# Optimization experiments

Measured on AMD Instinct MI355X. Metric: run time of the kernel, lower is better.

The kernel has to match this reference:

```python
import jax, jax.numpy as jnp
import numpy as np
import math

B, T, C, H = 2, 2048, 1024, 16

def setup_inputs() -> dict:
    key = jax.random.key(0)
    ks = jax.random.split(key, 5)
    s = 0.02
    return {
        "x": jax.random.normal(ks[0], (B, T, C), dtype=jnp.float32),
        "W_attn": jax.random.normal(ks[1], (C, 3 * C), dtype=jnp.float32) * s,
        "b_attn": jnp.zeros((3 * C,), dtype=jnp.float32),
        "W_proj": jax.random.normal(ks[2], (C, C), dtype=jnp.float32) * s,
        "b_proj": jnp.zeros((C,), dtype=jnp.float32),
    }

def reference(x, W_attn, b_attn, W_proj, b_proj):
    Bx, Tx, Cx = x.shape
    hd = Cx // H  # head dim = 64
    qkv = x @ W_attn + b_attn                      # [B,T,3C]
    q, k, v = jnp.split(qkv, 3, axis=-1)
    # [B,H,T,hd]
    q = q.reshape(Bx, Tx, H, hd).transpose(0, 2, 1, 3)
    k = k.reshape(Bx, Tx, H, hd).transpose(0, 2, 1, 3)
    v = v.reshape(Bx, Tx, H, hd).transpose(0, 2, 1, 3)
    scale = 1.0 / math.sqrt(hd)
    att = jnp.einsum('bhqd,bhkd->bhqk', q, k) * scale   # [B,H,T,T]
    causal = jnp.tril(jnp.ones((Tx, Tx), dtype=bool))
    att = jnp.where(causal[None, None, :, :], att, -jnp.inf)
    att = jax.nn.softmax(att, axis=-1)
    y = jnp.einsum('bhqk,bhkd->bhqd', att, v)           # [B,H,T,hd]
    y = y.transpose(0, 2, 1, 3).reshape(Bx, Tx, Cx)
    return y @ W_proj + b_proj
```

## Files before the change

### kernel.cpp

```cpp
#include <hip/hip_runtime.h>

typedef __attribute__((ext_vector_type(8))) __bf16 bf16x8;
typedef __attribute__((ext_vector_type(4))) float f32x4;

#define T_SEQ 2048
#define NH 16
#define HD 64
#define CDIM 1024
#define NQK 2048
#define NQKV 3072
#define MTOT 4096

#define SWZ(r, c) ((((r) * 8) + ((c) ^ ((r) & 7))) * 8)

__device__ __forceinline__ void async_load16(const void* g, void* l) {
    __builtin_amdgcn_global_load_lds(
        (const __attribute__((address_space(1))) void*)g,
        (__attribute__((address_space(3))) void*)l, 16, 0, 0);
}

__device__ __forceinline__ unsigned cvtpk_bf16(float lo, float hi) {
    unsigned r;
    asm("v_cvt_pk_bf16_f32 %0, %1, %2" : "=v"(r) : "v"(lo), "v"(hi));
    return r;
}
__device__ __forceinline__ void swap32(unsigned& a, unsigned& b) {
    asm("v_permlane32_swap_b32 %0, %1" : "+v"(a), "+v"(b));
}
__device__ __forceinline__ void swap16(unsigned& a, unsigned& b) {
    asm("v_permlane16_swap_b32 %0, %1" : "+v"(a), "+v"(b));
}

__global__ __launch_bounds__(256) void prep_kernel(
    const float* __restrict__ x, __bf16* __restrict__ xb,
    const float* __restrict__ Wa, const float* __restrict__ Wp,
    __bf16* __restrict__ WaT, __bf16* __restrict__ WpT) {
    __shared__ float tile[32][33];
    int bid = blockIdx.x;
    if (bid < 2048) {
        int i = (bid * 256 + threadIdx.x) * 8;
        float4 f0 = *(const float4*)(x + i);
        float4 f1 = *(const float4*)(x + i + 4);
        bf16x8 o;
        o[0] = (__bf16)f0.x; o[1] = (__bf16)f0.y; o[2] = (__bf16)f0.z; o[3] = (__bf16)f0.w;
        o[4] = (__bf16)f1.x; o[5] = (__bf16)f1.y; o[6] = (__bf16)f1.z; o[7] = (__bf16)f1.w;
        *(bf16x8*)(xb + i) = o;
        return;
    }
    int fb = bid - 2048;
    int bx = fb & 127, by = fb >> 7;
    const float* in; __bf16* out; int C;
    if (bx < 96) { in = Wa; out = WaT; C = 3072; }
    else         { in = Wp; out = WpT; C = 1024; bx -= 96; }
    int c0 = bx * 32, r0 = by * 32;
    int tx = threadIdx.x & 31, ty = threadIdx.x >> 5;
#pragma unroll
    for (int i = 0; i < 4; i++)
        tile[ty + i * 8][tx] = in[(size_t)(r0 + ty + i * 8) * C + c0 + tx];
    __syncthreads();
#pragma unroll
    for (int i = 0; i < 4; i++)
        out[(size_t)(c0 + ty + i * 8) * 1024 + r0 + tx] = (__bf16)tile[tx][ty + i * 8];
}

template <int WNW>
__global__ __launch_bounds__(256) void gemm_bt_kernel(
    const __bf16* __restrict__ A, const __bf16* __restrict__ Bt,
    const float* __restrict__ bias, int M, int N, int K, int mode,
    __bf16* __restrict__ qkb, __bf16* __restrict__ vtb, float* __restrict__ outf)
{
    constexpr int MI = (WNW == 2) ? 4 : 2;
    constexpr int BROWS = WNW * 64;
    __shared__ __bf16 As[128 * 64];
    __shared__ __bf16 Bs[BROWS * 64];

    int tid = threadIdx.x;
    int lane = tid & 63, wid = tid >> 6;
    int quad = lane >> 4, r16 = lane & 15;
    int wm = (WNW == 2) ? (wid >> 1) * 64 : wid * 32;
    int wn = (WNW == 2) ? (wid & 1) * 64 : 0;

    int id = blockIdx.y * gridDim.x + blockIdx.x;
    int nx = gridDim.x, ny = gridDim.y;
    int xcd = id & 7, wi = id >> 3;
    int cpx = nx >> 1;
    int rpx = ny >> 2;
    int rr = wi / cpx, cc = wi - rr * cpx;
    int bys = (xcd >> 1) * rpx + rr;
    int bxs = (xcd & 1) * cpx + cc;
    int bm = bys * 128, bn = bxs * (WNW * 64);

    f32x4 acc[MI][4] = {};

    int lrow = lane >> 3;
    int lcolsw = (((lane & 7) ^ (lrow & 7)) * 8);
    const __bf16* Ag = A + (size_t)(bm + wid * 32 + lrow) * K + lcolsw;
    const __bf16* Bg = Bt + (size_t)(bn + wid * (BROWS / 4) + lrow) * K + lcolsw;
    char* lA = (char*)As + wid * 4096;
    char* lB = (char*)Bs + wid * (BROWS / 4) * 128;

    for (int kt = 0; kt < K; kt += 64) {
        __syncthreads();
#pragma unroll
        for (int i = 0; i < 4; i++)
            async_load16(Ag + kt + (size_t)i * 8 * K, lA + i * 1024);
#pragma unroll
        for (int i = 0; i < BROWS / 32; i++)
            async_load16(Bg + kt + (size_t)i * 8 * K, lB + i * 1024);
        __syncthreads();
#pragma unroll
        for (int ks = 0; ks < 2; ks++) {
            bf16x8 af[MI], bfr[4];
#pragma unroll
            for (int i = 0; i < MI; i++)
                af[i] = *(const bf16x8*)&As[SWZ(wm + i * 16 + r16, ks * 4 + quad)];
#pragma unroll
            for (int i = 0; i < 4; i++)
                bfr[i] = *(const bf16x8*)&Bs[SWZ(wn + i * 16 + r16, ks * 4 + quad)];
#pragma unroll
            for (int mi = 0; mi < MI; mi++)
#pragma unroll
                for (int ni = 0; ni < 4; ni++)
                    acc[mi][ni] = __builtin_amdgcn_mfma_f32_16x16x32_bf16(
                        af[mi], bfr[ni], acc[mi][ni], 0, 0, 0);
        }
    }

    const float SC2 = 0.125f * 1.44269504088896f;
#pragma unroll
    for (int mi = 0; mi < MI; mi++) {
#pragma unroll
        for (int ni = 0; ni < 4; ni++) {
            int col = bn + wn + ni * 16 + r16;
            float bv = bias[col];
            int row0 = bm + wm + mi * 16 + quad * 4;
            if (mode == 1) {
#pragma unroll
                for (int rg = 0; rg < 4; rg++)
                    outf[(size_t)(row0 + rg) * N + col] = acc[mi][ni][rg] + bv;
            } else if (col < 1024) {
#pragma unroll
                for (int rg = 0; rg < 4; rg++)
                    qkb[(size_t)(row0 + rg) * NQK + col] = (__bf16)((acc[mi][ni][rg] + bv) * SC2);
            } else if (col < 2048) {
#pragma unroll
                for (int rg = 0; rg < 4; rg++)
                    qkb[(size_t)(row0 + rg) * NQK + col] = (__bf16)(acc[mi][ni][rg] + bv);
            } else {
                int dcol = col - 2048;
                int b = row0 >> 11, t0 = row0 & 2047;
                union { __bf16 h[4]; uint2 u; } pk;
#pragma unroll
                for (int rg = 0; rg < 4; rg++) pk.h[rg] = (__bf16)(acc[mi][ni][rg] + bv);
                *(uint2*)&vtb[((size_t)b * 1024 + dcol) * T_SEQ + t0] = pk.u;
            }
        }
    }
}

__global__ __launch_bounds__(256) void attn_kernel(
    const __bf16* __restrict__ qkb, const __bf16* __restrict__ vtb,
    __bf16* __restrict__ y1)
{
    __shared__ __bf16 Ks[2][64 * 64];
    __shared__ __bf16 Vs[2][64 * 64];

    int tid = threadIdx.x;
    int lane = tid & 63, w = tid >> 6;
    int quad = lane >> 4, r16 = lane & 15;
    int bh = blockIdx.y;
    int b = bh >> 4, h = bh & 15;
    int qtA = blockIdx.x, qtB = 31 - blockIdx.x;
    int qbA = qtA * 64, qbB = qtB * 64;

    const __bf16* Qh = qkb + (size_t)b * T_SEQ * NQK + h * HD;
    const __bf16* Kh = Qh + CDIM;
    const __bf16* Vh = vtb + ((size_t)b * 1024 + h * HD) * T_SEQ;

    const float NEG_INF = -__builtin_inff();
    int lrow = lane >> 3;
    int lcolsw = (((lane & 7) ^ (lrow & 7)) * 8);

    bf16x8 qfA[2], qfB[2];
#pragma unroll
    for (int ks = 0; ks < 2; ks++) {
        qfA[ks] = *(const bf16x8*)(Qh + (size_t)(qbA + w * 16 + r16) * NQK + ks * 32 + quad * 8);
        qfB[ks] = *(const bf16x8*)(Qh + (size_t)(qbB + w * 16 + r16) * NQK + ks * 32 + quad * 8);
    }

    bf16x8 onesv;
#pragma unroll
    for (int i = 0; i < 8; i++) onesv[i] = (__bf16)1.0f;

    f32x4 oA[4] = {}, oB[4] = {};
    f32x4 lA4 = {}, lB4 = {};
    int g0A = qbA + w * 16, g0B = qbB + w * 16;
    int qrowA = g0A + r16, qrowB = g0B + r16;

    auto stage = [&](int kt, int buf) {
        int kb = kt * 64;
        char* lK = (char*)Ks[buf] + w * 2048;
        char* lV = (char*)Vs[buf] + w * 2048;
        const __bf16* kg = Kh + (size_t)(kb + w * 16 + lrow) * NQK + lcolsw;
        const __bf16* vg = Vh + (size_t)(w * 16 + lrow) * T_SEQ + kb + lcolsw;
        async_load16(kg, lK);
        async_load16(kg + (size_t)8 * NQK, lK + 1024);
        async_load16(vg, lV);
        async_load16(vg + (size_t)8 * T_SEQ, lV + 1024);
    };

    auto softmax_xchg = [&](f32x4 (&s)[4], int qrow, int kb, bool diag,
                            bf16x8 (&pb)[2]) {
        if (diag) {
#pragma unroll
            for (int ni = 0; ni < 4; ni++)
#pragma unroll
                for (int rg = 0; rg < 4; rg++)
                    if (kb + ni * 16 + quad * 4 + rg > qrow) s[ni][rg] = NEG_INF;
        }
#pragma unroll
        for (int ni = 0; ni < 4; ni++)
#pragma unroll
            for (int rg = 0; rg < 4; rg++)
                s[ni][rg] = __builtin_amdgcn_exp2f(s[ni][rg]);
#pragma unroll
        for (int ks = 0; ks < 2; ks++) {
            unsigned X0 = cvtpk_bf16(s[2 * ks][0], s[2 * ks][1]);
            unsigned X1 = cvtpk_bf16(s[2 * ks][2], s[2 * ks][3]);
            unsigned Y0 = cvtpk_bf16(s[2 * ks + 1][0], s[2 * ks + 1][1]);
            unsigned Y1 = cvtpk_bf16(s[2 * ks + 1][2], s[2 * ks + 1][3]);
            swap32(X0, Y0); swap16(X0, Y0);
            swap32(X1, Y1); swap16(X1, Y1);
            union { unsigned u[4]; bf16x8 v; } pk;
            pk.u[0] = X0; pk.u[1] = X1; pk.u[2] = Y0; pk.u[3] = Y1;
            pb[ks] = pk.v;
        }
    };

    int nktA = qtA + 1, nktB = qtB + 1;
    stage(0, 0);
    int cur = 0;
    for (int kt = 0; kt < nktB; kt++) {
        __syncthreads();
        if (kt + 1 < nktB) stage(kt + 1, cur ^ 1);
        const bool doA = (kt < nktA);
        const int kb = kt * 64;

        f32x4 sB[4] = {}, sA[4] = {};
#pragma unroll
        for (int ks = 0; ks < 2; ks++) {
            bf16x8 kf[4];
#pragma unroll
            for (int ni = 0; ni < 4; ni++)
                kf[ni] = *(const bf16x8*)&Ks[cur][SWZ(ni * 16 + r16, ks * 4 + quad)];
            __builtin_amdgcn_s_setprio(1);
#pragma unroll
            for (int ni = 0; ni < 4; ni++)
                sB[ni] = __builtin_amdgcn_mfma_f32_16x16x32_bf16(kf[ni], qfB[ks], sB[ni], 0, 0, 0);
            if (doA) {
#pragma unroll
                for (int ni = 0; ni < 4; ni++)
                    sA[ni] = __builtin_amdgcn_mfma_f32_16x16x32_bf16(kf[ni], qfA[ks], sA[ni], 0, 0, 0);
            }
            __builtin_amdgcn_s_setprio(0);
        }

        bf16x8 pbB[2], pbA[2];
        softmax_xchg(sB, qrowB, kb, kb + 63 > g0B, pbB);
        if (doA) softmax_xchg(sA, qrowA, kb, kb + 63 > g0A, pbA);

#pragma unroll
        for (int ks = 0; ks < 2; ks++) {
            bf16x8 vf[4];
#pragma unroll
            for (int nd = 0; nd < 4; nd++)
                vf[nd] = *(const bf16x8*)&Vs[cur][SWZ(nd * 16 + r16, ks * 4 + quad)];
            __builtin_amdgcn_s_setprio(1);
#pragma unroll
            for (int nd = 0; nd < 4; nd++)
                oB[nd] = __builtin_amdgcn_mfma_f32_16x16x32_bf16(vf[nd], pbB[ks], oB[nd], 0, 0, 0);
            lB4 = __builtin_amdgcn_mfma_f32_16x16x32_bf16(onesv, pbB[ks], lB4, 0, 0, 0);
            __builtin_amdgcn_s_setprio(0);
            if (doA) {
                __builtin_amdgcn_s_setprio(1);
#pragma unroll
                for (int nd = 0; nd < 4; nd++)
                    oA[nd] = __builtin_amdgcn_mfma_f32_16x16x32_bf16(vf[nd], pbA[ks], oA[nd], 0, 0, 0);
                lA4 = __builtin_amdgcn_mfma_f32_16x16x32_bf16(onesv, pbA[ks], lA4, 0, 0, 0);
                __builtin_amdgcn_s_setprio(0);
            }
        }
        cur ^= 1;
    }

#pragma unroll
    for (int which = 0; which < 2; which++) {
        f32x4* o = which ? oB : oA;
        float inv = 1.f / (which ? lB4[0] : lA4[0]);
        int t = (which ? qbB : qbA) + w * 16 + r16;
#pragma unroll
        for (int nd = 0; nd < 4; nd++) {
            union { __bf16 h4[4]; uint2 u; } pk;
#pragma unroll
            for (int rg = 0; rg < 4; rg++) pk.h4[rg] = (__bf16)(o[nd][rg] * inv);
            *(uint2*)&y1[(size_t)(b * T_SEQ + t) * CDIM + h * HD + nd * 16 + quad * 4] = pk.u;
        }
    }
}

extern "C" void kernel_launch(void* const* d_in, const int* in_sizes, int n_in,
                              void* d_out, int out_size, void* d_ws, size_t ws_size,
                              hipStream_t stream) {
    const float* x = (const float*)d_in[0];
    const float* W_attn = (const float*)d_in[1];
    const float* b_attn = (const float*)d_in[2];
    const float* W_proj = (const float*)d_in[3];
    const float* b_proj = (const float*)d_in[4];
    float* out = (float*)d_out;

    char* p = (char*)d_ws;
    __bf16* xb = (__bf16*)p;   p += (size_t)MTOT * CDIM * 2;
    __bf16* WaT = (__bf16*)p;  p += (size_t)3 * CDIM * CDIM * 2;
    __bf16* WpT = (__bf16*)p;  p += (size_t)CDIM * CDIM * 2;
    __bf16* qkb = (__bf16*)p;  p += (size_t)MTOT * NQK * 2;
    __bf16* vtb = (__bf16*)p;  p += (size_t)2 * 1024 * T_SEQ * 2;
    __bf16* y1 = xb;

    prep_kernel<<<2048 + 4096, 256, 0, stream>>>(x, xb, W_attn, W_proj, WaT, WpT);
    gemm_bt_kernel<2><<<dim3(24, 32), 256, 0, stream>>>(xb, WaT, b_attn, MTOT, NQKV, CDIM,
                                                        0, qkb, vtb, nullptr);
    attn_kernel<<<dim3(16, 32), 256, 0, stream>>>(qkb, vtb, y1);
    gemm_bt_kernel<1><<<dim3(16, 32), 256, 0, stream>>>(y1, WpT, b_proj, MTOT, CDIM, CDIM,
                                                        1, nullptr, nullptr, out);
}
```

Baseline: 179.0 us.

## Double-buffer LDS tiles in GEMM to overlap global loads with MFMA

Splits the GEMM shared-memory A/B tiles into two buffers and prefetches the next K-tile with async global-to-LDS loads while the current tile is consumed by MFMA. Full __syncthreads pairs are replaced with explicit vmcnt waits and raw s_barrier calls, so load latency can overlap compute. This doubles LDS use per block, which may reduce occupancy, and relies on hand-counted vmcnt values matching the number of outstanding loads.

After: 187.1 us. +4.5%, slower.

```diff
diff --git a/kernel.cpp b/kernel.cpp
--- a/kernel.cpp
+++ b/kernel.cpp
@@ -71,8 +71,8 @@
 {
     constexpr int MI = (WNW == 2) ? 4 : 2;
     constexpr int BROWS = WNW * 64;
-    __shared__ __bf16 As[128 * 64];
-    __shared__ __bf16 Bs[BROWS * 64];
+    __shared__ __bf16 As[2][128 * 64];
+    __shared__ __bf16 Bs[2][BROWS * 64];
 
     int tid = threadIdx.x;
     int lane = tid & 63, wid = tid >> 6;
@@ -96,27 +96,46 @@
     int lcolsw = (((lane & 7) ^ (lrow & 7)) * 8);
     const __bf16* Ag = A + (size_t)(bm + wid * 32 + lrow) * K + lcolsw;
     const __bf16* Bg = Bt + (size_t)(bn + wid * (BROWS / 4) + lrow) * K + lcolsw;
-    char* lA = (char*)As + wid * 4096;
-    char* lB = (char*)Bs + wid * (BROWS / 4) * 128;
-
+
+    {
+        char* lA = (char*)As[0] + wid * 4096;
+        char* lB = (char*)Bs[0] + wid * (BROWS / 4) * 128;
+#pragma unroll
+        for (int i = 0; i < 4; i++)
+            async_load16(Ag + (size_t)i * 8 * K, lA + i * 1024);
+#pragma unroll
+        for (int i = 0; i < BROWS / 32; i++)
+            async_load16(Bg + (size_t)i * 8 * K, lB + i * 1024);
+    }
+
+    int buf = 0;
     for (int kt = 0; kt < K; kt += 64) {
-        __syncthreads();
-#pragma unroll
-        for (int i = 0; i < 4; i++)
-            async_load16(Ag + kt + (size_t)i * 8 * K, lA + i * 1024);
-#pragma unroll
-        for (int i = 0; i < BROWS / 32; i++)
-            async_load16(Bg + kt + (size_t)i * 8 * K, lB + i * 1024);
-        __syncthreads();
+        if (kt + 64 < K) {
+            char* lA = (char*)As[buf ^ 1] + wid * 4096;
+            char* lB = (char*)Bs[buf ^ 1] + wid * (BROWS / 4) * 128;
+#pragma unroll
+            for (int i = 0; i < 4; i++)
+                async_load16(Ag + kt + 64 + (size_t)i * 8 * K, lA + i * 1024);
+#pragma unroll
+            for (int i = 0; i < BROWS / 32; i++)
+                async_load16(Bg + kt + 64 + (size_t)i * 8 * K, lB + i * 1024);
+            if constexpr (WNW == 2) asm volatile("s_waitcnt vmcnt(8)" ::: "memory");
+            else                    asm volatile("s_waitcnt vmcnt(6)" ::: "memory");
+        } else {
+            asm volatile("s_waitcnt vmcnt(0)" ::: "memory");
+        }
+        __builtin_amdgcn_s_barrier();
+        __builtin_amdgcn_sched_barrier(0);
+
 #pragma unroll
         for (int ks = 0; ks < 2; ks++) {
             bf16x8 af[MI], bfr[4];
 #pragma unroll
             for (int i = 0; i < MI; i++)
-                af[i] = *(const bf16x8*)&As[SWZ(wm + i * 16 + r16, ks * 4 + quad)];
+                af[i] = *(const bf16x8*)&As[buf][SWZ(wm + i * 16 + r16, ks * 4 + quad)];
 #pragma unroll
             for (int i = 0; i < 4; i++)
-                bfr[i] = *(const bf16x8*)&Bs[SWZ(wn + i * 16 + r16, ks * 4 + quad)];
+                bfr[i] = *(const bf16x8*)&Bs[buf][SWZ(wn + i * 16 + r16, ks * 4 + quad)];
 #pragma unroll
             for (int mi = 0; mi < MI; mi++)
 #pragma unroll
@@ -124,6 +143,8 @@
                     acc[mi][ni] = __builtin_amdgcn_mfma_f32_16x16x32_bf16(
                         af[mi], bfr[ni], acc[mi][ni], 0, 0, 0);
         }
+        __builtin_amdgcn_s_barrier();
+        buf ^= 1;
     }
 
     const float SC2 = 0.125f * 1.44269504088896f;
```
